# Optimization experiments

Hardware: AMD Instinct MI355X
Metric: run time of the kernel (lower is better)

Reference implementation:

```python
import jax, jax.numpy as jnp
import numpy as np

N_ENT = 50000
N_REL = 500
N_EDGE = 800000
D_IN = 100
D_OUT = 100
ALPHA = 0.2  # LeakyReLU negative slope


def setup_inputs() -> dict:
    key = jax.random.key(0)
    k0, k1, k2, k3, k4 = jax.random.split(key, 5)
    entity_embedding = jax.random.normal(k0, (N_ENT, D_IN), dtype=jnp.float32) * 0.1
    relation_embedding = jax.random.normal(k1, (N_REL, D_IN), dtype=jnp.float32) * 0.1
    W = jax.random.normal(k2, (D_IN, D_OUT), dtype=jnp.float32) * 0.1
    edge_index = jax.random.randint(k3, (2, N_EDGE), 0, N_ENT, dtype=jnp.int32)
    edge_type = jax.random.randint(k4, (N_EDGE,), 0, N_REL, dtype=jnp.int32)
    return {
        "entity_embedding": entity_embedding,
        "relation_embedding": relation_embedding,
        "W": W,
        "edge_index": edge_index,
        "edge_type": edge_type,
    }


def reference(entity_embedding, relation_embedding, W, edge_index, edge_type):
    N = entity_embedding.shape[0]
    # project input embeddings with shared W (in_features -> out_features)
    ent = entity_embedding @ W          # [N_ent, D]
    rel = relation_embedding @ W        # [N_rel, D]

    h = edge_index[0]                   # destination / head nodes [E]
    t = edge_index[1]                   # source / tail nodes      [E]

    # TransE edge score: ||h + r - t||_2 per edge
    diff = ent[h] + rel[edge_type] - ent[t]          # [E, D]
    score = jnp.sqrt(jnp.sum(diff * diff, axis=1))   # [E]
    e = jax.nn.leaky_relu(score, negative_slope=ALPHA)

    # scatter-softmax over edges grouped by head node
    seg_max = jax.ops.segment_max(e, h, num_segments=N)         # [N]
    seg_max = jnp.where(jnp.isfinite(seg_max), seg_max, 0.0)    # empty segments -> -inf
    ex = jnp.exp(e - seg_max[h])                                 # [E]
    denom = jax.ops.segment_sum(ex, h, num_segments=N)          # [N]
    att = ex / (denom[h] + 1e-16)                                # [E]

    # message: composition 'sub' of tail embedding and relation, weighted by attention
    msg = (ent[t] - rel[edge_type]) * att[:, None]               # [E, D]
    out = jax.ops.segment_sum(msg, h, num_segments=N)            # [N, D]

    # concat=True -> nonlinearity (ELU, standard GAT behavior)
    return jax.nn.elu(out)
```

## Files before the change

### kernel.cpp

```cpp
#include <hip/hip_runtime.h>
#include <math.h>

#define N_ENT  50000
#define N_REL  500
#define N_EDGE 800000
#define D      100
#define ALPHA  0.2f

#define SCAN_B 256
#define NBLK_SCAN ((N_ENT + SCAN_B - 1) / SCAN_B)

#define PROJ_TPB  256
#define PROJ_RPB  50
#define PROJ_RPT  25
#define WT_STRIDE 101
#define ENT_BLKS  (N_ENT / PROJ_RPB)
#define REL_BLKS  (N_REL / PROJ_RPB)

__global__ __launch_bounds__(PROJ_TPB) void proj_kernel(const float* __restrict__ Xe,
                                                        const float* __restrict__ Xr,
                                                        const float* __restrict__ W,
                                                        float* __restrict__ Ye,
                                                        float* __restrict__ Yr,
                                                        int* __restrict__ deg) {
    __shared__ float WT[D * WT_STRIDE];
    __shared__ float Xs[PROJ_RPB * D];
    int t = threadIdx.x;

    const float* X; float* Y; size_t xbase;
    if (blockIdx.x < ENT_BLKS) {
        X = Xe; Y = Ye; xbase = (size_t)blockIdx.x * PROJ_RPB * D;
    } else {
        X = Xr; Y = Yr; xbase = (size_t)(blockIdx.x - ENT_BLKS) * PROJ_RPB * D;
    }

    for (int i = t; i < D * D; i += PROJ_TPB) {
        int k = i / D, c = i % D;
        WT[c * WT_STRIDE + k] = W[i];
    }
    for (int i = t; i < PROJ_RPB * D; i += PROJ_TPB)
        Xs[i] = X[xbase + i];
    __syncthreads();

    if (t < 200) {
        int c  = t % 100;
        int r0 = (t / 100) * PROJ_RPT;
        const float* wt = &WT[c * WT_STRIDE];
        for (int j = 0; j < PROJ_RPT; j += 5) {
            const float* x0 = &Xs[(r0 + j    ) * D];
            const float* x1 = &Xs[(r0 + j + 1) * D];
            const float* x2 = &Xs[(r0 + j + 2) * D];
            const float* x3 = &Xs[(r0 + j + 3) * D];
            const float* x4 = &Xs[(r0 + j + 4) * D];
            float a0 = 0.f, a1 = 0.f, a2 = 0.f, a3 = 0.f, a4 = 0.f;
            #pragma unroll
            for (int k = 0; k < D; ++k) {
                float w = wt[k];
                a0 = fmaf(x0[k], w, a0);
                a1 = fmaf(x1[k], w, a1);
                a2 = fmaf(x2[k], w, a2);
                a3 = fmaf(x3[k], w, a3);
                a4 = fmaf(x4[k], w, a4);
            }
            Y[xbase + (size_t)(r0 + j    ) * D + c] = a0;
            Y[xbase + (size_t)(r0 + j + 1) * D + c] = a1;
            Y[xbase + (size_t)(r0 + j + 2) * D + c] = a2;
            Y[xbase + (size_t)(r0 + j + 3) * D + c] = a3;
            Y[xbase + (size_t)(r0 + j + 4) * D + c] = a4;
        }
    } else {
        int j = blockIdx.x * (PROJ_TPB - 200) + (t - 200);
        if (j < N_ENT) deg[j] = 0;
    }
}

__global__ void degree_kernel(const int* __restrict__ h_idx, int* __restrict__ deg) {
    int e = blockIdx.x * blockDim.x + threadIdx.x;
    if (e < N_EDGE) atomicAdd(&deg[h_idx[e]], 1);
}

__global__ void scan1_kernel(const int* __restrict__ deg, int* __restrict__ bsum) {
    __shared__ int s[SCAN_B];
    int i = blockIdx.x * SCAN_B + threadIdx.x;
    s[threadIdx.x] = (i < N_ENT) ? deg[i] : 0;
    __syncthreads();
    for (int off = SCAN_B / 2; off; off >>= 1) {
        if (threadIdx.x < off) s[threadIdx.x] += s[threadIdx.x + off];
        __syncthreads();
    }
    if (threadIdx.x == 0) bsum[blockIdx.x] = s[0];
}

__global__ void scan2_kernel(const int* __restrict__ bsum, int* __restrict__ boff) {
    __shared__ int s[SCAN_B];
    int tid = threadIdx.x;
    int v = (tid < NBLK_SCAN) ? bsum[tid] : 0;
    s[tid] = v;
    __syncthreads();
    for (int off = 1; off < SCAN_B; off <<= 1) {
        int x = (tid >= off) ? s[tid - off] : 0;
        __syncthreads();
        s[tid] += x;
        __syncthreads();
    }
    if (tid < NBLK_SCAN) boff[tid] = s[tid] - v;
}

__global__ void scan3_kernel(const int* __restrict__ deg, const int* __restrict__ boff,
                             int* __restrict__ rowptr, int* __restrict__ cursor) {
    __shared__ int s[SCAN_B];
    int tid = threadIdx.x;
    int i = blockIdx.x * SCAN_B + tid;
    int v = (i < N_ENT) ? deg[i] : 0;
    s[tid] = v;
    __syncthreads();
    for (int off = 1; off < SCAN_B; off <<= 1) {
        int x = (tid >= off) ? s[tid - off] : 0;
        __syncthreads();
        s[tid] += x;
        __syncthreads();
    }
    int excl = s[tid] - v + boff[blockIdx.x];
    if (i < N_ENT) { rowptr[i] = excl; cursor[i] = excl; }
    if (i == N_ENT - 1) rowptr[N_ENT] = excl + v;
}

__global__ void fill_kernel(const int* __restrict__ h_idx, const int* __restrict__ t_idx,
                            const int* __restrict__ etype, int* __restrict__ cursor,
                            int2* __restrict__ tr_sorted) {
    int e = blockIdx.x * blockDim.x + threadIdx.x;
    if (e >= N_EDGE) return;
    int h = h_idx[e];
    int pos = atomicAdd(&cursor[h], 1);
    tr_sorted[pos] = make_int2(t_idx[e], etype[e]);
}

__device__ __forceinline__ float edge_reduce32(const float4& eh, const float4& v) {
    float dx = eh.x + v.x, dy = eh.y + v.y, dz = eh.z + v.z, dw = eh.w + v.w;
    float s = dx * dx;
    s = fmaf(dy, dy, s);
    s = fmaf(dz, dz, s);
    s = fmaf(dw, dw, s);
    #pragma unroll
    for (int off = 16; off; off >>= 1) s += __shfl_xor(s, off, 32);
    return sqrtf(s);
}

__device__ __forceinline__ void online_update(float sc, const float4& v,
                                              float& m, float& den, float4& acc) {
    float d  = sc - m;
    float e  = __expf(-fabsf(d));
    float scale = (d >= 0.f) ? e : 1.f;
    float ex    = (d >= 0.f) ? 1.f : e;
    m = fmaxf(m, sc);
    den   = den * scale + ex;
    acc.x = acc.x * scale - v.x * ex;
    acc.y = acc.y * scale - v.y * ex;
    acc.z = acc.z * scale - v.z * ex;
    acc.w = acc.w * scale - v.w * ex;
}

__global__ __launch_bounds__(256) void fused_kernel(const float* __restrict__ ent,
                                                    const float* __restrict__ rel,
                                                    const int* __restrict__ rowptr,
                                                    const int2* __restrict__ tr_sorted,
                                                    float* __restrict__ out) {
    int head = blockIdx.x * 8 + (threadIdx.x >> 5);
    int lane = threadIdx.x & 31;
    if (head >= N_ENT) return;
    int beg = rowptr[head], end = rowptr[head + 1];

    float4 eh = make_float4(0.f, 0.f, 0.f, 0.f);
    if (lane < 25) eh = ((const float4*)(ent + (size_t)head * D))[lane];

    float  m   = -INFINITY;
    float  den = 0.f;
    float4 acc = make_float4(0.f, 0.f, 0.f, 0.f);

    int i = beg;
    for (; i + 1 < end; i += 2) {
        int2 e0 = tr_sorted[i];
        int2 e1 = tr_sorted[i + 1];
        float4 v0 = make_float4(0.f, 0.f, 0.f, 0.f);
        float4 v1 = make_float4(0.f, 0.f, 0.f, 0.f);
        if (lane < 25) {
            float4 et0 = ((const float4*)(ent + (size_t)e0.x * D))[lane];
            float4 er0 = ((const float4*)(rel + (size_t)e0.y * D))[lane];
            float4 et1 = ((const float4*)(ent + (size_t)e1.x * D))[lane];
            float4 er1 = ((const float4*)(rel + (size_t)e1.y * D))[lane];
            v0 = make_float4(er0.x - et0.x, er0.y - et0.y, er0.z - et0.z, er0.w - et0.w);
            v1 = make_float4(er1.x - et1.x, er1.y - et1.y, er1.z - et1.z, er1.w - et1.w);
        }
        float sc0 = edge_reduce32(eh, v0);
        float sc1 = edge_reduce32(eh, v1);
        online_update(sc0, v0, m, den, acc);
        online_update(sc1, v1, m, den, acc);
    }
    if (i < end) {
        int2 e0 = tr_sorted[i];
        float4 v = make_float4(0.f, 0.f, 0.f, 0.f);
        if (lane < 25) {
            float4 et = ((const float4*)(ent + (size_t)e0.x * D))[lane];
            float4 er = ((const float4*)(rel + (size_t)e0.y * D))[lane];
            v = make_float4(er.x - et.x, er.y - et.y, er.z - et.z, er.w - et.w);
        }
        float sc = edge_reduce32(eh, v);
        online_update(sc, v, m, den, acc);
    }

    float inv = 1.f / (den + 1e-16f);
    float ox = acc.x * inv, oy = acc.y * inv, oz = acc.z * inv, ow = acc.w * inv;
    ox = ox > 0.f ? ox : expm1f(ox);
    oy = oy > 0.f ? oy : expm1f(oy);
    oz = oz > 0.f ? oz : expm1f(oz);
    ow = ow > 0.f ? ow : expm1f(ow);
    if (lane < 25)
        ((float4*)(out + (size_t)head * D))[lane] = make_float4(ox, oy, oz, ow);
}

extern "C" void kernel_launch(void* const* d_in, const int* in_sizes, int n_in,
                              void* d_out, int out_size, void* d_ws, size_t ws_size,
                              hipStream_t stream) {
    const float* entity_emb = (const float*)d_in[0];
    const float* rel_emb    = (const float*)d_in[1];
    const float* W          = (const float*)d_in[2];
    const int*   edge_index = (const int*)d_in[3];
    const int*   edge_type  = (const int*)d_in[4];
    float*       out        = (float*)d_out;

    const int* h_idx = edge_index;
    const int* t_idx = edge_index + N_EDGE;

    float* ent       = (float*)d_ws;
    float* rel       = ent + (size_t)N_ENT * D;
    int*   deg       = (int*)(rel + (size_t)N_REL * D);
    int*   rowptr    = deg + N_ENT;
    int*   cursor    = rowptr + (N_ENT + 1);
    int*   bsum      = cursor + N_ENT;
    int*   boff      = bsum + SCAN_B;
    int2*  tr_sorted = (int2*)(boff + SCAN_B);

    proj_kernel<<<ENT_BLKS + REL_BLKS, PROJ_TPB, 0, stream>>>(entity_emb, rel_emb,
                                                              W, ent, rel, deg);

    degree_kernel<<<(N_EDGE + 255) / 256, 256, 0, stream>>>(h_idx, deg);
    scan1_kernel<<<NBLK_SCAN, SCAN_B, 0, stream>>>(deg, bsum);
    scan2_kernel<<<1, SCAN_B, 0, stream>>>(bsum, boff);
    scan3_kernel<<<NBLK_SCAN, SCAN_B, 0, stream>>>(deg, boff, rowptr, cursor);
    fill_kernel<<<(N_EDGE + 255) / 256, 256, 0, stream>>>(h_idx, t_idx, edge_type,
                                                          cursor, tr_sorted);

    fused_kernel<<<N_ENT / 8, 256, 0, stream>>>(ent, rel, rowptr, tr_sorted, out);
}
```

Before: 263.0 us.

## Hold W columns in registers and split K across two wavefronts in projection

```diff
diff --git a/kernel.cpp b/kernel.cpp
--- a/kernel.cpp
+++ b/kernel.cpp
@@ -12,8 +12,6 @@
 
 #define PROJ_TPB  256
 #define PROJ_RPB  50
-#define PROJ_RPT  25
-#define WT_STRIDE 101
 #define ENT_BLKS  (N_ENT / PROJ_RPB)
 #define REL_BLKS  (N_REL / PROJ_RPB)
 
@@ -23,8 +21,8 @@
                                                         float* __restrict__ Ye,
                                                         float* __restrict__ Yr,
                                                         int* __restrict__ deg) {
-    __shared__ float WT[D * WT_STRIDE];
     __shared__ float Xs[PROJ_RPB * D];
+    __shared__ float P[5][D];
     int t = threadIdx.x;
 
     const float* X; float* Y; size_t xbase;
@@ -34,43 +32,69 @@
         X = Xr; Y = Yr; xbase = (size_t)(blockIdx.x - ENT_BLKS) * PROJ_RPB * D;
     }
 
-    for (int i = t; i < D * D; i += PROJ_TPB) {
-        int k = i / D, c = i % D;
-        WT[c * WT_STRIDE + k] = W[i];
-    }
+    int half, c;
+    if (t < 100)                { half = 0; c = t; }
+    else if (t >= 128 && t < 228) { half = 1; c = t - 128; }
+    else                        { half = -1; c = 0; }
+
+    if (half < 0) {
+        int idx = (t < 128) ? (t - 100) : (28 + (t - 228));
+        int j = blockIdx.x * 56 + idx;
+        if (j < N_ENT) deg[j] = 0;
+    }
+
     for (int i = t; i < PROJ_RPB * D; i += PROJ_TPB)
         Xs[i] = X[xbase + i];
-    __syncthreads();
-
-    if (t < 200) {
-        int c  = t % 100;
-        int r0 = (t / 100) * PROJ_RPT;
-        const float* wt = &WT[c * WT_STRIDE];
-        for (int j = 0; j < PROJ_RPT; j += 5) {
-            const float* x0 = &Xs[(r0 + j    ) * D];
-            const float* x1 = &Xs[(r0 + j + 1) * D];
-            const float* x2 = &Xs[(r0 + j + 2) * D];
-            const float* x3 = &Xs[(r0 + j + 3) * D];
-            const float* x4 = &Xs[(r0 + j + 4) * D];
-            float a0 = 0.f, a1 = 0.f, a2 = 0.f, a3 = 0.f, a4 = 0.f;
-            #pragma unroll
-            for (int k = 0; k < D; ++k) {
-                float w = wt[k];
-                a0 = fmaf(x0[k], w, a0);
-                a1 = fmaf(x1[k], w, a1);
-                a2 = fmaf(x2[k], w, a2);
-                a3 = fmaf(x3[k], w, a3);
-                a4 = fmaf(x4[k], w, a4);
+
+    float w[52];
+    if (half == 0) {
+        #pragma unroll
+        for (int k = 0; k < 52; ++k) w[k] = W[k * D + c];
+    } else if (half == 1) {
+        #pragma unroll
+        for (int k = 0; k < 48; ++k) w[k] = W[(52 + k) * D + c];
+    }
+    __syncthreads();
+
+    for (int g = 0; g < 10; ++g) {
+        int r0 = g * 5;
+        float a[5] = {0.f, 0.f, 0.f, 0.f, 0.f};
+        if (half == 0) {
+            #pragma unroll
+            for (int r = 0; r < 5; ++r) {
+                const float4* xr = (const float4*)&Xs[(r0 + r) * D];
+                #pragma unroll
+                for (int q = 0; q < 13; ++q) {
+                    float4 xv = xr[q];
+                    a[r] = fmaf(xv.x, w[4*q    ], a[r]);
+                    a[r] = fmaf(xv.y, w[4*q + 1], a[r]);
+                    a[r] = fmaf(xv.z, w[4*q + 2], a[r]);
+                    a[r] = fmaf(xv.w, w[4*q + 3], a[r]);
+                }
             }
-            Y[xbase + (size_t)(r0 + j    ) * D + c] = a0;
-            Y[xbase + (size_t)(r0 + j + 1) * D + c] = a1;
-            Y[xbase + (size_t)(r0 + j + 2) * D + c] = a2;
-            Y[xbase + (size_t)(r0 + j + 3) * D + c] = a3;
-            Y[xbase + (size_t)(r0 + j + 4) * D + c] = a4;
-        }
-    } else {
-        int j = blockIdx.x * (PROJ_TPB - 200) + (t - 200);
-        if (j < N_ENT) deg[j] = 0;
+        } else if (half == 1) {
+            #pragma unroll
+            for (int r = 0; r < 5; ++r) {
+                const float4* xr = (const float4*)&Xs[(r0 + r) * D] + 13;
+                #pragma unroll
+                for (int q = 0; q < 12; ++q) {
+                    float4 xv = xr[q];
+                    a[r] = fmaf(xv.x, w[4*q    ], a[r]);
+                    a[r] = fmaf(xv.y, w[4*q + 1], a[r]);
+                    a[r] = fmaf(xv.z, w[4*q + 2], a[r]);
+                    a[r] = fmaf(xv.w, w[4*q + 3], a[r]);
+                }
+            }
+            #pragma unroll
+            for (int r = 0; r < 5; ++r) P[r][c] = a[r];
+        }
+        __syncthreads();
+        if (half == 0) {
+            #pragma unroll
+            for (int r = 0; r < 5; ++r)
+                Y[xbase + (size_t)(r0 + r) * D + c] = a[r] + P[r][c];
+        }
+        __syncthreads();
     }
 }
 
```

Result: no change. 266.2 us (+1.2%).
